# Kernel optimization log

Hardware: AMD Instinct MI355X
Metric: run time of the kernel (lower is better)

The kernel has to match this reference:

```python
import jax, jax.numpy as jnp
import numpy as np

T, N, E, IN, HID, H, DK, L, OUT = 2, 16384, 262144, 128, 256, 8, 32, 2, 64
SRC_T, DST_T = (0, 1), (1, 0)
SQRT_DK = float(np.sqrt(DK))


def _gelu(x):
    return jax.nn.gelu(x, approximate=False)


def _seg_softmax(scores, seg, n):
    # edge softmax normalized by destination node (variable in-degree segments)
    m = jax.ops.segment_max(scores, seg, num_segments=n)
    e = jnp.exp(scores - m[seg])
    d = jax.ops.segment_sum(e, seg, num_segments=n)
    return e / d[seg]


def _posvect(x, ww, wb, lw, lb, sw, sb, gw, gb, fw, fb):
    # x: [T,N,6] scalar features; per-(type,modality) weights [T,6,HID]; fw: [T,6,4*HID,HID]
    xe = x[..., None]                                    # [T,N,6,1]
    aff = lambda w, b: xe * w[:, None] + b[:, None]      # [T,N,6,HID]
    acts = (jnp.sin(aff(ww, wb)), aff(lw, lb),
            jax.nn.softplus(aff(sw, sb)), jax.nn.sigmoid(aff(gw, gb)))
    out = fb[:, None]
    for i, a in enumerate(acts):
        out = out + jnp.einsum('tnmh,tmhk->tnmk', a, fw[:, :, i * HID:(i + 1) * HID, :])
    return out                                           # [T,N,6,HID]


def _forward(node_ft, scalars, src_idx, dst_idx, proj_w, proj_b,
             pv_wave_w, pv_wave_b, pv_lin_w, pv_lin_b, pv_sp_w, pv_sp_b,
             pv_sig_w, pv_sig_b, pv_fc_w, pv_fc_b, ima_w1, ima_b1, ima_w2,
             lyr_k_w, lyr_q_w, lyr_v_w, lyr_fc_w, lyr_k_b, lyr_q_b, lyr_v_b,
             lyr_fc_b, lyr_att_w, lyr_val_w, lyr_canon, lyr_res,
             lyr_ln_g, lyr_ln_b, out_w, out_b, sel_node_type):
    # per-type input projection + six positional encodings -> 7 modalities
    h0 = _gelu(jnp.einsum('tnd,tdh->tnh', node_ft, proj_w) + proj_b[:, None])
    pv = _gelu(_posvect(scalars, pv_wave_w, pv_wave_b, pv_lin_w, pv_lin_b,
                        pv_sp_w, pv_sp_b, pv_sig_w, pv_sig_b, pv_fc_w, pv_fc_b))
    z = jnp.concatenate([h0[:, :, None], pv], axis=2)    # [T,N,7,HID]
    w = jnp.tanh(z @ ima_w1 + ima_b1) @ ima_w2           # [T,N,7,1]
    h = (jax.nn.softmax(w, axis=2) * z).sum(2)           # [T,N,HID]
    for l in range(L):
        k = (jnp.einsum('tnd,tdh->tnh', h, lyr_k_w[l]) + lyr_k_b[l][:, None]).reshape(T, N, H, DK)
        q = (jnp.einsum('tnd,tdh->tnh', h, lyr_q_w[l]) + lyr_q_b[l][:, None]).reshape(T, N, H, DK)
        v = (jnp.einsum('tnd,tdh->tnh', h, lyr_v_w[l]) + lyr_v_b[l][:, None]).reshape(T, N, H, DK)
        agg = [None, None]
        for e in range(2):  # canonical etypes: (a->b), (b->a)
            st, dt = SRC_T[e], DST_T[e]
            ke = jnp.einsum('nhi,hij->nhj', k[st], lyr_att_w[l, e])
            ve = jnp.einsum('nhi,hij->nhj', v[st], lyr_val_w[l, e])
            s, d = src_idx[e], dst_idx[e]
            score = (q[dt][d] * ke[s]).sum(-1) * lyr_canon[l, e] / SQRT_DK  # [E,H]
            attn = _seg_softmax(score, d, N)
            agg[dt] = jax.ops.segment_sum(ve[s] * attn[..., None], d, num_segments=N)
        t = jnp.stack(agg).reshape(T, N, HID)  # cross_reducer mean over single etype per dst == identity
        alpha = jax.nn.sigmoid(lyr_res[l])[:, None, None]
        hp = jnp.einsum('tnh,thk->tnk', t, lyr_fc_w[l]) + lyr_fc_b[l][:, None]
        hp = hp * alpha + h * (1.0 - alpha)
        mu = hp.mean(-1, keepdims=True)
        var = ((hp - mu) ** 2).mean(-1, keepdims=True)
        h = (hp - mu) / jnp.sqrt(var + 1e-5) * lyr_ln_g[l][:, None] + lyr_ln_b[l][:, None]
    return h[sel_node_type] @ out_w + out_b


def setup_inputs() -> dict:
    key = jax.random.key(0)
    ks = iter(jax.random.split(key, 64))
    nrm = lambda shape, scale=1.0: jax.random.normal(next(ks), shape, dtype=jnp.float32) * scale
    inp = {}
    inp['node_ft'] = nrm((T, N, IN))
    inp['scalars'] = jax.random.uniform(next(ks), (T, N, 6), dtype=jnp.float32)
    inp['src_idx'] = jax.random.randint(next(ks), (T, E), 0, N, dtype=jnp.int32)
    inp['dst_idx'] = jax.random.randint(next(ks), (T, E), 0, N, dtype=jnp.int32)
    inp['proj_w'] = nrm((T, IN, HID), IN ** -0.5)
    inp['proj_b'] = jnp.zeros((T, HID), jnp.float32)
    for nm in ['pv_wave_w', 'pv_wave_b', 'pv_lin_w', 'pv_lin_b', 'pv_sp_w', 'pv_sp_b', 'pv_sig_w', 'pv_sig_b']:
        inp[nm] = nrm((T, 6, HID))
    inp['pv_fc_w'] = nrm((T, 6, 4 * HID, HID), (4 * HID) ** -0.5)
    inp['pv_fc_b'] = jnp.zeros((T, 6, HID), jnp.float32)
    inp['ima_w1'] = nrm((HID, 128), HID ** -0.5)
    inp['ima_b1'] = jnp.zeros((128,), jnp.float32)
    inp['ima_w2'] = nrm((128, 1), 128 ** -0.5)
    for nm in ['lyr_k_w', 'lyr_q_w', 'lyr_v_w', 'lyr_fc_w']:
        inp[nm] = nrm((L, T, HID, HID), HID ** -0.5)
    for nm in ['lyr_k_b', 'lyr_q_b', 'lyr_v_b', 'lyr_fc_b']:
        inp[nm] = jnp.zeros((L, T, HID), jnp.float32)
    inp['lyr_att_w'] = nrm((L, 2, H, DK, DK), DK ** -0.5)
    inp['lyr_val_w'] = nrm((L, 2, H, DK, DK), DK ** -0.5)
    inp['lyr_canon'] = jnp.ones((L, 2, H), jnp.float32)
    inp['lyr_res'] = jnp.ones((L, T), jnp.float32)
    inp['lyr_ln_g'] = jnp.ones((L, T, HID), jnp.float32)
    inp['lyr_ln_b'] = jnp.zeros((L, T, HID), jnp.float32)
    inp['out_w'] = nrm((HID, OUT), HID ** -0.5)
    inp['out_b'] = jnp.zeros((OUT,), jnp.float32)
    inp['sel_node_type'] = 0
    return inp


def reference(node_ft, scalars, src_idx, dst_idx, proj_w, proj_b,
              pv_wave_w, pv_wave_b, pv_lin_w, pv_lin_b, pv_sp_w, pv_sp_b,
              pv_sig_w, pv_sig_b, pv_fc_w, pv_fc_b, ima_w1, ima_b1, ima_w2,
              lyr_k_w, lyr_q_w, lyr_v_w, lyr_fc_w, lyr_k_b, lyr_q_b, lyr_v_b,
              lyr_fc_b, lyr_att_w, lyr_val_w, lyr_canon, lyr_res,
              lyr_ln_g, lyr_ln_b, out_w, out_b, sel_node_type):
    return _forward(node_ft, scalars, src_idx, dst_idx, proj_w, proj_b,
                    pv_wave_w, pv_wave_b, pv_lin_w, pv_lin_b, pv_sp_w, pv_sp_b,
                    pv_sig_w, pv_sig_b, pv_fc_w, pv_fc_b, ima_w1, ima_b1, ima_w2,
                    lyr_k_w, lyr_q_w, lyr_v_w, lyr_fc_w, lyr_k_b, lyr_q_b, lyr_v_b,
                    lyr_fc_b, lyr_att_w, lyr_val_w, lyr_canon, lyr_res,
                    lyr_ln_g, lyr_ln_b, out_w, out_b, sel_node_type)
```

## Files before the change

### kernel.cpp

```cpp
#include <hip/hip_runtime.h>
#include <hip/hip_bf16.h>

typedef unsigned short u16;
typedef unsigned int   u32;
typedef __attribute__((ext_vector_type(8))) short bf16x8;
typedef __attribute__((ext_vector_type(4))) float f32x4;
typedef __attribute__((ext_vector_type(4))) u16   u16x4;

constexpr int TT  = 2;
constexpr int NN  = 16384;
constexpr int EE  = 262144;

__device__ __forceinline__ u16 f2b(float f){
  u32 x = __float_as_uint(f);
  u32 r = (x + 0x7fffu + ((x >> 16) & 1u)) >> 16;
  return (u16)r;
}
__device__ __forceinline__ float b2f(u16 u){ return __uint_as_float(((u32)u) << 16); }
__device__ __forceinline__ u32 pack2bf(float a, float b){
  __hip_bfloat162 h = __float22bfloat162_rn(make_float2(a, b));
  union { __hip_bfloat162 h2; u32 u; } cv; cv.h2 = h; return cv.u;
}

__device__ __forceinline__ int swz64(int row, int c){
  return (row << 6) + (c ^ ((row & 7) << 3));
}

__device__ __forceinline__ void gl_lds16(const u16* g, u16* l){
  __builtin_amdgcn_global_load_lds(
      (const __attribute__((address_space(1))) u32*)g,
      (__attribute__((address_space(3))) u32*)l, 16, 0, 0);
}

__device__ __forceinline__ float fast_tanh(float u){
  return 1.f - 2.f*__builtin_amdgcn_rcpf(1.f + __expf(2.f*u));
}
__device__ __forceinline__ float gelu_f(float x){
  float u = 0.7978845608028654f * (x + 0.044715f * x*x*x);
  return 0.5f * x * (1.f + fast_tanh(u));
}

__global__ void csr_hist(const int* __restrict__ dst, int* __restrict__ cnt){
  int id = blockIdx.x*256 + threadIdx.x;
  int e = id >> 18;
  atomicAdd(&cnt[e*NN + dst[id]], 1);
}

__global__ void csr_scan(const int* __restrict__ cnt, int* __restrict__ offs){
  const int e = blockIdx.x, tid = threadIdx.x;
  const int CH = NN/256;
  const int* c = cnt + e*NN;
  int* of = offs + e*(NN+1);
  const int base = tid*CH;
  int s = 0;
  for(int i=0;i<CH;i++) s += c[base+i];
  __shared__ int sm[256];
  sm[tid] = s; __syncthreads();
  for(int o=1;o<256;o<<=1){
    int v = (tid>=o) ? sm[tid-o] : 0;
    __syncthreads();
    sm[tid] += v;
    __syncthreads();
  }
  int run = sm[tid] - s;
  for(int i=0;i<CH;i++){ of[base+i] = run; run += c[base+i]; }
  if(tid==255) of[NN] = run;
}

__global__ void csr_scatter(const int* __restrict__ dst, const int* __restrict__ src,
                            const int* __restrict__ offs, int* __restrict__ cur,
                            int* __restrict__ elist){
  int id = blockIdx.x*256 + threadIdx.x;
  int e = id >> 18;
  int d = dst[id];
  int pos = offs[e*(NN+1)+d] + atomicAdd(&cur[e*NN+d], 1);
  elist[e*EE + pos] = src[id];
}

__global__ void tconv(const float* __restrict__ in, u16* __restrict__ out, int K, int Nc){
  __shared__ float tile[32][33];
  const long base = (long)blockIdx.z * K * Nc;
  const int k0 = blockIdx.x*32, n0 = blockIdx.y*32;
  const int tx = threadIdx.x, ty = threadIdx.y;
  for(int i=0;i<32;i+=8)
    tile[ty+i][tx] = in[base + (long)(k0+ty+i)*Nc + n0+tx];
  __syncthreads();
  for(int i=0;i<32;i+=8)
    out[base + (long)(n0+ty+i)*K + k0+tx] = f2b(tile[tx][ty+i]);
}

__global__ void eff_w(const float* __restrict__ kw, const float* __restrict__ vw,
                      const float* __restrict__ kb, const float* __restrict__ vb,
                      const float* __restrict__ att, const float* __restrict__ val,
                      u16* __restrict__ qkvwt, float* __restrict__ qkvb){
  const int h = blockIdx.x, lt = blockIdx.y, kv = blockIdx.z;
  const int l = lt >> 1;
  const float* W = (kv ? vw : kw) + (long)lt*65536;
  const float* A = (kv ? val : att) + (long)lt*8192 + h*1024;
  const float* B = (kv ? vb : kb) + (long)lt*256 + h*32;
  __shared__ float As[32][33];
  for(int idx=threadIdx.x; idx<1024; idx+=256) As[idx>>5][idx&31] = A[idx];
  __syncthreads();
  const int r = threadIdx.x;
  float x[32];
  const float* wr = W + (long)r*256 + h*32;
  #pragma unroll
  for(int i=0;i<32;i++) x[i] = wr[i];
  u16* outb = qkvwt + (kv ? 524288 : 0) + (long)lt*65536;
  #pragma unroll 4
  for(int j=0;j<32;j++){
    float s = 0.f;
    #pragma unroll
    for(int i=0;i<32;i++) s = fmaf(x[i], As[i][j], s);
    outb[(h*32 + j)*256 + r] = f2b(s);
  }
  if (r < 32){
    float s = 0.f;
    #pragma unroll
    for(int i=0;i<32;i++) s = fmaf(B[i], As[i][r], s);
    qkvb[l*1536 + (kv ? 1024 : 0) + (lt&1)*256 + h*32 + r] = s;
  }
}

__global__ void pack_qb(const float* __restrict__ qb, float* __restrict__ qkvb){
  int i = blockIdx.x*256 + threadIdx.x;
  int l = i >> 9, r = i & 511;
  qkvb[l*1536 + 512 + r] = qb[l*512 + r];
}

__global__ void cheb_g(const float* __restrict__ ww, const float* __restrict__ wb,
                       const float* __restrict__ lw, const float* __restrict__ lb,
                       const float* __restrict__ sw, const float* __restrict__ sb,
                       const float* __restrict__ gw, const float* __restrict__ gb,
                       const float* __restrict__ fcw, float* __restrict__ Gpart){
  const int p  = blockIdx.x;
  const int by = blockIdx.y;
  const int zg = blockIdx.z;
  const int s  = p >> 1;
  const int tid = threadIdx.x;
  __shared__ float as_[128][9];
  if (tid < 128){
    const int hl = (p & 1)*128 + tid;
    const float* W = (s==0 ? ww : s==1 ? lw : s==2 ? sw : gw) + by*256;
    const float* B = (s==0 ? wb : s==1 ? lb : s==2 ? sb : gb) + by*256;
    const float w = W[hl], b = B[hl];
    #pragma unroll
    for (int dd=0; dd<8; dd++){
      const int d = zg*8 + dd;
      const float th = ((float)d + 0.5f) * (3.14159265358979323846f/32.f);
      const float x  = 0.5f*cosf(th) + 0.5f;
      const float y  = x*w + b;
      float a;
      if (s==0)      a = sinf(y);
      else if (s==1) a = y;
      else if (s==2) a = fmaxf(y,0.f) + log1pf(expf(-fabsf(y)));
      else           a = 1.f/(1.f + expf(-y));
      as_[tid][dd] = a;
    }
  }
  __syncthreads();
  const int k = tid;
  float acc[8];
  #pragma unroll
  for (int dd=0; dd<8; dd++) acc[dd] = 0.f;
  const float* fwp = fcw + ((long)by*1024 + p*128)*256 + k;
  for (int hh=0; hh<128; hh++){
    const float f = fwp[(long)hh*256];
    #pragma unroll
    for (int dd=0; dd<8; dd++) acc[dd] = fmaf(as_[hh][dd], f, acc[dd]);
  }
  float* gp = Gpart + (long)(by*8 + p)*32*256 + (long)(zg*8)*256 + k;
  #pragma unroll
  for (int dd=0; dd<8; dd++) gp[dd*256] = acc[dd];
}

__global__ void cheb_dct(const float* __restrict__ Gpart, const float* __restrict__ fcb,
                         u16* __restrict__ Cbf, float* __restrict__ c0b){
  const int by = blockIdx.x; const int k = threadIdx.x;
  __shared__ float ct[1024];
  for (int i=k; i<1024; i+=256){
    const int j = i>>5, d = i&31;
    ct[i] = cosf((float)j*((float)d + 0.5f)*(3.14159265358979323846f/32.f));
  }
  __syncthreads();
  float g[32];
  #pragma unroll
  for (int d=0; d<32; d++){
    float s = 0.f;
    #pragma unroll
    for (int p=0; p<8; p++) s += Gpart[(long)(by*8+p)*32*256 + d*256 + k];
    g[d] = s;
  }
  u16* co = Cbf + ((long)by*256 + k)*32;
  #pragma unroll
  for (int j=0; j<32; j++){
    float s = 0.f;
    #pragma unroll
    for (int d=0; d<32; d++) s = fmaf(g[d], ct[j*32+d], s);
    if (j==0){ c0b[by*256+k] = s*(1.f/32.f) + fcb[by*256+k]; co[0] = 0; }
    else co[j] = f2b(s*(1.f/16.f));
  }
}

__global__ void __launch_bounds__(256,2)
posvect2(const float* __restrict__ scalars, const u16* __restrict__ Cbf,
         const float* __restrict__ c0b, u16* __restrict__ zb){
  __shared__ __align__(16) u16 lB[256*40];
  __shared__ float xs[128];
  const int tid = threadIdx.x;
  const int by = blockIdx.y;
  const int t = by / 6, m = by % 6;
  const int m0 = blockIdx.x * 128;
  const int lane = tid & 63, wvi = tid >> 6;
  const int wc0 = wvi * 64;
  const int l16 = lane & 15, qd = lane >> 4;

  if (tid < 128) xs[tid] = scalars[((long)t*NN + m0 + tid)*6 + m];
  const u16* Cb = Cbf + (long)by*8192;
  for (int idx = tid; idx < 1024; idx += 256){
    const int row = idx >> 2, ch = idx & 3;
    *(uint4*)&lB[row*40 + ch*8] = *(const uint4*)&Cb[row*32 + ch*8];
  }
  __syncthreads();

  bf16x8 af[8];
  #pragma unroll
  for (int i=0;i<8;i++){
    const float u = 2.f*xs[i*16 + l16] - 1.f;
    float t0 = 1.f, t1 = u;
    u32 pk[16];
    pk[0] = pack2bf(t0, t1);
    #pragma unroll
    for (int j2=1; j2<16; j2++){
      const float a = 2.f*u*t1 - t0;
      const float b = 2.f*u*a  - t1;
      pk[j2] = pack2bf(a, b);
      t0 = a; t1 = b;
    }
    u32 w[4];
    #pragma unroll
    for (int c=0;c<4;c++){
      const u32 v01 = (qd & 2) ? pk[8+c]  : pk[c];
      const u32 v23 = (qd & 2) ? pk[12+c] : pk[4+c];
      w[c] = (qd & 1) ? v23 : v01;
    }
    union { u32 u4[4]; bf16x8 v; } cv;
    cv.u4[0]=w[0]; cv.u4[1]=w[1]; cv.u4[2]=w[2]; cv.u4[3]=w[3];
    af[i] = cv.v;
  }

  bf16x8 bfr[4];
  #pragma unroll
  for (int jj=0;jj<4;jj++)
    bfr[jj] = *(const bf16x8*)&lB[(wc0 + jj*16 + l16)*40 + qd*8];

  f32x4 acc[8][4];
  #pragma unroll
  for (int i=0;i<8;i++)
    #pragma unroll
    for (int jj=0;jj<4;jj++)
      acc[i][jj] = __builtin_amdgcn_mfma_f32_16x16x32_bf16(
          af[i], bfr[jj], (f32x4){0.f,0.f,0.f,0.f}, 0,0,0);

  float bvj[4];
  #pragma unroll
  for (int jj=0;jj<4;jj++) bvj[jj] = c0b[by*256 + wc0 + jj*16 + l16];

  u16* st = (u16*)lB;
  u16* zout = zb + ((long)t*NN + m0)*1792 + (m+1)*256;
  #pragma unroll
  for (int c=0;c<4;c++){
    __syncthreads();
    #pragma unroll
    for (int ii=0;ii<2;ii++){
      const int i = c*2 + ii;
      #pragma unroll
      for (int jj=0;jj<4;jj++){
        const int col = wc0 + jj*16 + l16;
        #pragma unroll
        for (int r=0;r<4;r++){
          const int rowl = ii*16 + qd*4 + r;
          st[rowl*264 + col] = f2b(gelu_f(acc[i][jj][r] + bvj[jj]));
        }
      }
    }
    __syncthreads();
    #pragma unroll
    for (int it=0; it<4; it++){
      const int f = it*256 + tid;
      const int rowl = f >> 5, seg = f & 31;
      const uint4 v = *(const uint4*)&st[rowl*264 + seg*8];
      *(uint4*)&zout[(long)(c*32 + rowl)*1792 + seg*8] = v;
    }
  }
}

template<int BM,int BN,int BK,int WM,int WN,int ASRC,int EPI,int ZQKV>
__global__ void __launch_bounds__(256,2)
gemm_k(const void* __restrict__ Av, const u16* __restrict__ Bt,
       const float* __restrict__ bias, void* Cv,
       int K, int lda, int ldc,
       long strideA, long strideB, long strideBias, long strideC,
       const float* resid, const float* __restrict__ resgate,
       const int* __restrict__ selp, u16* __restrict__ kvout,
       const float* __restrict__ lng, const float* __restrict__ lnb)
{
  static_assert(BK == 64, "swizzle assumes BK=64");
  constexpr int WTM = BM/WM, WTN = BN/WN;
  constexpr int RM = WTM/16, RN = WTN/16;
  __shared__ __align__(16) u16 lA[BM*64];
  __shared__ __align__(16) u16 lB[BN*64];

  const int tid = threadIdx.x;
  const int by  = blockIdx.y;
  const int m0  = blockIdx.x * BM;
  const int lane = tid & 63, wvi = tid >> 6;
  const int wr = wvi / WN, wc = wvi % WN;
  const int wr0 = wr * WTM, wc0 = wc * WTN;
  const int l16 = lane & 15, qd = lane >> 4;
  const int csrc = (((lane & 7) ^ (lane >> 3)) << 3);

  int zq = 0; int boff = 0;
  if constexpr (ZQKV){
    zq = blockIdx.z;
    boff = zq*512;
  }

  long aoff = (long)by * strideA;
  if (selp) aoff += (long)selp[0] * strideA;
  const float* A32 = (const float*)Av;
  const u16*   A16 = (const u16*)Av;
  const u16*   Bp  = Bt + (long)by * strideB + (long)zq * 262144;

  f32x4 acc[RM][RN];
  #pragma unroll
  for(int i=0;i<RM;i++)
    #pragma unroll
    for(int j=0;j<RN;j++) acc[i][j] = (f32x4){0.f,0.f,0.f,0.f};

  for(int k0=0;k0<K;k0+=BK){
    if constexpr (ASRC == 0){
      for(int idx=tid; idx < BM*16; idx += 256){
        int r = idx >> 4, c = (idx & 15)*4;
        const float4 v = *(const float4*)(A32 + aoff + (long)(m0+r)*lda + k0 + c);
        uint2 o2; o2.x = pack2bf(v.x, v.y); o2.y = pack2bf(v.z, v.w);
        *(uint2*)&lA[swz64(r, c)] = o2;
      }
    } else {
      #pragma unroll
      for(int ch = wvi; ch < BM/8; ch += 4){
        const int r = ch*8 + (lane>>3);
        gl_lds16(A16 + aoff + (long)(m0+r)*lda + k0 + csrc, &lA[ch*512]);
      }
    }
    #pragma unroll
    for(int ch = wvi; ch < BN/8; ch += 4){
      const int n = ch*8 + (lane>>3);
      gl_lds16(Bp + (long)n*K + k0 + csrc, &lB[ch*512]);
    }
    __syncthreads();
    #pragma unroll
    for(int ks=0; ks<BK; ks+=32){
      bf16x8 af[RM], bfr[RN];
      #pragma unroll
      for(int i=0;i<RM;i++) af[i]  = *(const bf16x8*)&lA[swz64(wr0 + i*16 + l16, ks + qd*8)];
      #pragma unroll
      for(int j=0;j<RN;j++) bfr[j] = *(const bf16x8*)&lB[swz64(wc0 + j*16 + l16, ks + qd*8)];
      #pragma unroll
      for(int i=0;i<RM;i++)
        #pragma unroll
        for(int j=0;j<RN;j++)
          acc[i][j] = __builtin_amdgcn_mfma_f32_16x16x32_bf16(af[i], bfr[j], acc[i][j], 0,0,0);
    }
    __syncthreads();
  }

  if constexpr (EPI == 4){
    float* rsum = (float*)lA;
    #pragma unroll
    for(int i=0;i<RM;i++){
      #pragma unroll
      for(int r=0;r<4;r++){
        float part = 0.f;
        #pragma unroll
        for(int jj=0;jj<RN;jj++){
          const int col = wc0 + jj*16 + l16;
          const float v = fast_tanh(acc[i][jj][r] + bias[boff + col]);
          part += v * resid[col];
        }
        part += __shfl_xor(part,1); part += __shfl_xor(part,2);
        part += __shfl_xor(part,4); part += __shfl_xor(part,8);
        if (l16 == 0) rsum[wc*BM + wr0 + i*16 + qd*4 + r] = part;
      }
    }
    __syncthreads();
    if (tid < BM){
      float s = 0.f;
      #pragma unroll
      for(int w=0;w<WN;w++) s += rsum[w*BM + tid];
      ((float*)Cv)[m0 + tid] = s;
    }
    return;
  } else if constexpr (EPI == 5){
    float* red1 = (float*)lA;
    float* red2 = red1 + WN*BM;
    float* muv  = red2 + WN*BM;
    const float alpha = 1.f/(1.f + __expf(-resgate[by]));
    #pragma unroll
    for(int i=0;i<RM;i++){
      #pragma unroll
      for(int r=0;r<4;r++){
        const int rloc = wr0 + i*16 + qd*4 + r;
        const int row = m0 + rloc;
        float s1 = 0.f, s2 = 0.f;
        #pragma unroll
        for(int j=0;j<RN;j++){
          const int col = wc0 + j*16 + l16;
          float v = acc[i][j][r] + bias[(long)by*strideBias + col];
          const float hv = resid[(long)by*strideC + (long)row*ldc + col];
          v = v*alpha + hv*(1.f - alpha);
          acc[i][j][r] = v;
          s1 += v; s2 += v*v;
        }
        s1 += __shfl_xor(s1,1); s1 += __shfl_xor(s1,2); s1 += __shfl_xor(s1,4); s1 += __shfl_xor(s1,8);
        s2 += __shfl_xor(s2,1); s2 += __shfl_xor(s2,2); s2 += __shfl_xor(s2,4); s2 += __shfl_xor(s2,8);
        if (l16 == 0){ red1[wc*BM + rloc] = s1; red2[wc*BM + rloc] = s2; }
      }
    }
    __syncthreads();
    if (tid < BM){
      float s1 = 0.f, s2 = 0.f;
      #pragma unroll
      for(int w=0;w<WN;w++){ s1 += red1[w*BM + tid]; s2 += red2[w*BM + tid]; }
      const float mu = s1*(1.f/256.f);
      const float var = s2*(1.f/256.f) - mu*mu;
      muv[tid*2]   = mu;
      muv[tid*2+1] = rsqrtf(fmaxf(var, 0.f) + 1e-5f);
    }
    __syncthreads();
    #pragma unroll
    for(int i=0;i<RM;i++){
      #pragma unroll
      for(int r=0;r<4;r++){
        const int rloc = wr0 + i*16 + qd*4 + r;
        const int row = m0 + rloc;
        const float mu = muv[rloc*2], rs = muv[rloc*2+1];
        #pragma unroll
        for(int j=0;j<RN;j++){
          const int col = wc0 + j*16 + l16;
          const float o = (acc[i][j][r]-mu)*rs*lng[by*256+col] + lnb[by*256+col];
          ((float*)Cv)[(long)by*strideC + (long)row*ldc + col] = o;
        }
      }
    }
    return;
  } else {
    #pragma unroll
    for(int i=0;i<RM;i++){
      #pragma unroll
      for(int j=0;j<RN;j++){
        const int col = wc0 + j*16 + l16;
        const float bv = bias[(long)by*strideBias + boff + col];
        #pragma unroll
        for(int r=0;r<4;r++){
          const int row = m0 + wr0 + i*16 + qd*4 + r;
          float v = acc[i][j][r] + bv;
          if constexpr (ZQKV){
            if (zq == 1)
              ((u16*)Cv)[(long)by*strideC + (long)row*ldc + col] = f2b(v);
            else
              kvout[((long)by*NN + row)*512 + ((col>>2)<<3) + (zq==2 ? 4 : 0) + (col&3)] = f2b(v);
          } else {
            const long cidx = (long)by*strideC + (long)row*ldc + col;
            if constexpr (EPI == 0) ((float*)Cv)[cidx] = v;
            else ((u16*)Cv)[cidx] = f2b(gelu_f(v));
          }
        }
      }
    }
  }
}

__global__ void ima_combine(const u16* __restrict__ zb, const float* __restrict__ wbuf,
                            float* __restrict__ H){
  const int row = blockIdx.x*4 + (threadIdx.x>>6);
  const int lane = threadIdx.x & 63;
  const float* w7 = wbuf + (long)row*7;
  float w[7]; float mx = -1e30f;
  #pragma unroll
  for(int m=0;m<7;m++){ w[m] = w7[m]; mx = fmaxf(mx, w[m]); }
  float sum = 0.f;
  #pragma unroll
  for(int m=0;m<7;m++){ w[m] = __expf(w[m]-mx); sum += w[m]; }
  const float inv = __builtin_amdgcn_rcpf(sum);
  float4 acc = {0,0,0,0};
  #pragma unroll
  for(int m=0;m<7;m++){
    const u16x4 z4 = *(const u16x4*)&zb[((long)row*7 + m)*256 + lane*4];
    const float p = w[m]*inv;
    acc.x += p*b2f(z4.x); acc.y += p*b2f(z4.y); acc.z += p*b2f(z4.z); acc.w += p*b2f(z4.w);
  }
  *(float4*)&H[(long)row*256 + lane*4] = acc;
}

__global__ void attn_agg(const u16* __restrict__ Q16, const u16* __restrict__ KV,
                         u16* __restrict__ AGG,
                         const int* __restrict__ offs, const int* __restrict__ elist,
                         const float* __restrict__ canon){
  const int e = blockIdx.y, dt = 1 - e;
  const int d = blockIdx.x*4 + (threadIdx.x>>6);
  const int lane = threadIdx.x & 63;
  const float scale = canon[e*8 + (lane>>3)] * 0.17677669529663687f;

  const uint2 qv = *(const uint2*)&Q16[((long)dt*NN + d)*256 + lane*4];
  const float q0 = b2f((u16)(qv.x&0xffff)), q1 = b2f((u16)(qv.x>>16));
  const float q2 = b2f((u16)(qv.y&0xffff)), q3 = b2f((u16)(qv.y>>16));

  const int p0 = offs[e*(NN+1) + d], p1 = offs[e*(NN+1) + d + 1];
  const int* el = elist + (long)e*EE;
  const u16* KVb = KV + (long)e*NN*512;

  float a0=0.f, a1=0.f, a2=0.f, a3=0.f;
  float den = 0.f;

  auto process = [&](const uint4 kv){
    float dp = q0*b2f((u16)(kv.x&0xffff)) + q1*b2f((u16)(kv.x>>16))
             + q2*b2f((u16)(kv.y&0xffff)) + q3*b2f((u16)(kv.y>>16));
    dp += __shfl_xor(dp,1); dp += __shfl_xor(dp,2); dp += __shfl_xor(dp,4);
    const float w = __expf(dp*scale);
    den += w;
    a0 = fmaf(w, b2f((u16)(kv.z&0xffff)), a0);
    a1 = fmaf(w, b2f((u16)(kv.z>>16)),    a1);
    a2 = fmaf(w, b2f((u16)(kv.w&0xffff)), a2);
    a3 = fmaf(w, b2f((u16)(kv.w>>16)),    a3);
  };

  int p = p0;
  for(; p+8 <= p1; p += 8){
    uint4 kv[8];
    #pragma unroll
    for(int u=0;u<8;u++) kv[u] = *(const uint4*)&KVb[(long)el[p+u]*512 + lane*8];
    #pragma unroll
    for(int u=0;u<8;u++) process(kv[u]);
  }
  for(; p+2 <= p1; p += 2){
    const uint4 a = *(const uint4*)&KVb[(long)el[p]*512 + lane*8];
    const uint4 b = *(const uint4*)&KVb[(long)el[p+1]*512 + lane*8];
    process(a); process(b);
  }
  if (p < p1){
    const uint4 a = *(const uint4*)&KVb[(long)el[p]*512 + lane*8];
    process(a);
  }

  uint2 o = {0,0};
  if (p1 > p0){
    const float r = 1.f/den;
    o.x = pack2bf(a0*r, a1*r);
    o.y = pack2bf(a2*r, a3*r);
  }
  *(uint2*)&AGG[((long)dt*NN + d)*256 + lane*4] = o;
}

extern "C" void kernel_launch(void* const* d_in, const int* in_sizes, int n_in,
                              void* d_out, int out_size, void* d_ws, size_t ws_size,
                              hipStream_t stream) {
  const float* node_ft = (const float*)d_in[0];
  const float* scalars = (const float*)d_in[1];
  const int*   src_idx = (const int*)d_in[2];
  const int*   dst_idx = (const int*)d_in[3];
  const float* proj_w  = (const float*)d_in[4];
  const float* proj_b  = (const float*)d_in[5];
  const float* pv_ww   = (const float*)d_in[6];
  const float* pv_wb   = (const float*)d_in[7];
  const float* pv_lw   = (const float*)d_in[8];
  const float* pv_lb   = (const float*)d_in[9];
  const float* pv_sw   = (const float*)d_in[10];
  const float* pv_sb   = (const float*)d_in[11];
  const float* pv_gw   = (const float*)d_in[12];
  const float* pv_gb   = (const float*)d_in[13];
  const float* pv_fcw  = (const float*)d_in[14];
  const float* pv_fcb  = (const float*)d_in[15];
  const float* ima_w1  = (const float*)d_in[16];
  const float* ima_b1  = (const float*)d_in[17];
  const float* ima_w2  = (const float*)d_in[18];
  const float* lyr_k_w = (const float*)d_in[19];
  const float* lyr_q_w = (const float*)d_in[20];
  const float* lyr_v_w = (const float*)d_in[21];
  const float* lyr_fc_w= (const float*)d_in[22];
  const float* lyr_k_b = (const float*)d_in[23];
  const float* lyr_q_b = (const float*)d_in[24];
  const float* lyr_v_b = (const float*)d_in[25];
  const float* lyr_fc_b= (const float*)d_in[26];
  const float* lyr_att_w=(const float*)d_in[27];
  const float* lyr_val_w=(const float*)d_in[28];
  const float* lyr_canon=(const float*)d_in[29];
  const float* lyr_res = (const float*)d_in[30];
  const float* lyr_ln_g= (const float*)d_in[31];
  const float* lyr_ln_b= (const float*)d_in[32];
  const float* out_w   = (const float*)d_in[33];
  const float* out_b   = (const float*)d_in[34];
  const int*   sel     = (const int*)d_in[35];
  float* outp = (float*)d_out;

  char* ws = (char*)d_ws;
  size_t o = 0;
  auto alloc = [&](size_t bytes)->char*{ char* p = ws + o; o = (o + bytes + 255) & ~(size_t)255; return p; };

  int*   cnt    = (int*)  alloc(2*NN*4);
  int*   cur    = (int*)  alloc(2*NN*4);
  int*   offs   = (int*)  alloc(2*(NN+1)*4);
  int*   elist  = (int*)  alloc(2*EE*4);
  u16*   projwt = (u16*)  alloc((size_t)TT*128*256*2);
  u16*   imaw1t = (u16*)  alloc((size_t)256*128*2);
  u16*   qkvwt  = (u16*)  alloc((size_t)3*262144*2);
  u16*   fcwt   = (u16*)  alloc((size_t)4*256*256*2);
  u16*   outwt  = (u16*)  alloc((size_t)64*256*2);
  float* hbuf   = (float*)alloc((size_t)TT*NN*256*4);
  float* wbuf   = (float*)alloc((size_t)TT*NN*7*4);
  float* Gpart  = (float*)alloc((size_t)12*8*32*256*4);
  u16*   Cbf    = (u16*)  alloc((size_t)12*256*32*2);
  float* c0b    = (float*)alloc((size_t)12*256*4);
  float* qkvb   = (float*)alloc((size_t)TT*3*2*256*4);
  char*  arena  = alloc((size_t)176160768);
  if (o > ws_size) return;

  u16*   zbuf  = (u16*)arena;
  u16*   Qb16  = (u16*)arena;
  u16*   KVb   = (u16*)(arena + 16777216);
  u16*   AGG16 = (u16*)(arena + 50331648);

  hipMemsetAsync(cnt, 0, 2*NN*4, stream);
  hipMemsetAsync(cur, 0, 2*NN*4, stream);
  csr_hist   <<<2*EE/256, 256, 0, stream>>>(dst_idx, cnt);
  csr_scan   <<<2, 256, 0, stream>>>(cnt, offs);
  csr_scatter<<<2*EE/256, 256, 0, stream>>>(dst_idx, src_idx, offs, cur, elist);

  tconv<<<dim3( 4,8, 2), dim3(32,8), 0, stream>>>(proj_w,   projwt, 128, 256);
  tconv<<<dim3( 8,4, 1), dim3(32,8), 0, stream>>>(ima_w1,   imaw1t, 256, 128);
  tconv<<<dim3( 8,8, 4), dim3(32,8), 0, stream>>>(lyr_q_w,  qkvwt + 262144, 256, 256);
  tconv<<<dim3( 8,8, 4), dim3(32,8), 0, stream>>>(lyr_fc_w, fcwt,   256, 256);
  tconv<<<dim3( 8,2, 1), dim3(32,8), 0, stream>>>(out_w,    outwt,  256, 64);
  eff_w<<<dim3(8,4,2), 256, 0, stream>>>(lyr_k_w, lyr_v_w, lyr_k_b, lyr_v_b,
                                         lyr_att_w, lyr_val_w, qkvwt, qkvb);
  pack_qb<<<4, 256, 0, stream>>>(lyr_q_b, qkvb);

  cheb_g  <<<dim3(8,12,4), 256, 0, stream>>>(pv_ww, pv_wb, pv_lw, pv_lb,
                                             pv_sw, pv_sb, pv_gw, pv_gb, pv_fcw, Gpart);
  cheb_dct<<<12, 256, 0, stream>>>(Gpart, pv_fcb, Cbf, c0b);

  gemm_k<64,256,64,1,4,0,1,0><<<dim3(256,TT), 256, 0, stream>>>(
      node_ft, projwt, proj_b, zbuf, 128, 128, 1792,
      (long)NN*128, 32768L, 256L, (long)NN*1792, nullptr, nullptr, nullptr, nullptr,
      nullptr, nullptr);

  posvect2<<<dim3(128,12), 256, 0, stream>>>(scalars, Cbf, c0b, zbuf);

  gemm_k<64,128,64,2,2,1,4,0><<<dim3(3584,1), 256, 0, stream>>>(
      zbuf, imaw1t, ima_b1, wbuf, 256, 256, 0,
      0L, 0L, 0L, 0L, ima_w2, nullptr, nullptr, nullptr, nullptr, nullptr);
  ima_combine<<<TT*NN/4, 256, 0, stream>>>(zbuf, wbuf, hbuf);

  for (int l = 0; l < 2; ++l){
    gemm_k<64,256,64,1,4,0,0,1><<<dim3(256,TT,3), 256, 0, stream>>>(
        hbuf, qkvwt + (size_t)l*131072, qkvb + (size_t)l*1536, Qb16, 256, 256, 256,
        (long)NN*256, 65536L, 256L, (long)NN*256, nullptr, nullptr, nullptr, KVb,
        nullptr, nullptr);

    attn_agg<<<dim3(NN/4, 2), 256, 0, stream>>>(Qb16, KVb, AGG16, offs, elist,
                                                lyr_canon + l*2*8);

    gemm_k<64,256,64,1,4,1,5,0><<<dim3(256,TT), 256, 0, stream>>>(
        AGG16, fcwt + (size_t)l*2*65536, lyr_fc_b + l*2*256, hbuf, 256, 256, 256,
        (long)NN*256, 65536L, 256L, (long)NN*256, hbuf, lyr_res + l*2, nullptr, nullptr,
        lyr_ln_g + l*2*256, lyr_ln_b + l*2*256);
  }

  gemm_k<256,64,64,4,1,0,0,0><<<dim3(64,1), 256, 0, stream>>>(
      hbuf, outwt, out_b, outp, 256, 256, 64,
      (long)NN*256, 0L, 0L, 0L, nullptr, nullptr, sel, nullptr, nullptr, nullptr);

  (void)in_sizes; (void)n_in; (void)out_size;
}
```

Baseline: 661.9 us.

## Interleave K/V weight columns at pack time and use one-wave attention blocks

The K and V effective weights and biases are now written in an interleaved column order during weight packing, so the QKV GEMM epilogue stores KV contiguously instead of scattering each column through an index remap. Weights are regrouped per (layer,type) as [K|V|Q], and Q moves to z=2. The aggregation kernel is relaunched with one 64-thread wave per destination node instead of four waves per block, aiming for finer-grained scheduling of variable-degree nodes. Risk: bias and weight index remapping must match exactly, and smaller blocks add launch and occupancy overhead.

```diff
diff --git a/kernel.cpp b/kernel.cpp
--- a/kernel.cpp
+++ b/kernel.cpp
@@ -77,16 +77,18 @@
   elist[e*EE + pos] = src[id];
 }
 
-__global__ void tconv(const float* __restrict__ in, u16* __restrict__ out, int K, int Nc){
+__global__ void tconv(const float* __restrict__ in, u16* __restrict__ out, int K, int Nc,
+                      long ozstride){
   __shared__ float tile[32][33];
-  const long base = (long)blockIdx.z * K * Nc;
+  const long ibase = (long)blockIdx.z * K * Nc;
+  const long obase = (long)blockIdx.z * ozstride;
   const int k0 = blockIdx.x*32, n0 = blockIdx.y*32;
   const int tx = threadIdx.x, ty = threadIdx.y;
   for(int i=0;i<32;i+=8)
-    tile[ty+i][tx] = in[base + (long)(k0+ty+i)*Nc + n0+tx];
+    tile[ty+i][tx] = in[ibase + (long)(k0+ty+i)*Nc + n0+tx];
   __syncthreads();
   for(int i=0;i<32;i+=8)
-    out[base + (long)(n0+ty+i)*K + k0+tx] = f2b(tile[tx][ty+i]);
+    out[obase + (long)(n0+ty+i)*K + k0+tx] = f2b(tile[tx][ty+i]);
 }
 
 __global__ void eff_w(const float* __restrict__ kw, const float* __restrict__ vw,
@@ -106,26 +108,30 @@
   const float* wr = W + (long)r*256 + h*32;
   #pragma unroll
   for(int i=0;i<32;i++) x[i] = wr[i];
-  u16* outb = qkvwt + (kv ? 524288 : 0) + (long)lt*65536;
+  u16* outb = qkvwt + (long)lt*196608;
   #pragma unroll 4
   for(int j=0;j<32;j++){
     float s = 0.f;
     #pragma unroll
     for(int i=0;i<32;i++) s = fmaf(x[i], As[i][j], s);
-    outb[(h*32 + j)*256 + r] = f2b(s);
+    const int c = h*32 + j;
+    const int mc = ((c>>2)<<3) + kv*4 + (c&3);
+    outb[(long)mc*256 + r] = f2b(s);
   }
   if (r < 32){
     float s = 0.f;
     #pragma unroll
     for(int i=0;i<32;i++) s = fmaf(B[i], As[i][r], s);
-    qkvb[l*1536 + (kv ? 1024 : 0) + (lt&1)*256 + h*32 + r] = s;
+    const int c = h*32 + r;
+    const int mc = ((c>>2)<<3) + kv*4 + (c&3);
+    qkvb[l*1536 + (lt&1)*512 + mc] = s;
   }
 }
 
 __global__ void pack_qb(const float* __restrict__ qb, float* __restrict__ qkvb){
   int i = blockIdx.x*256 + threadIdx.x;
   int l = i >> 9, r = i & 511;
-  qkvb[l*1536 + 512 + r] = qb[l*512 + r];
+  qkvb[l*1536 + 1024 + r] = qb[l*512 + r];
 }
 
 __global__ void cheb_g(const float* __restrict__ ww, const float* __restrict__ wb,
@@ -320,17 +326,14 @@
   const int l16 = lane & 15, qd = lane >> 4;
   const int csrc = (((lane & 7) ^ (lane >> 3)) << 3);
 
-  int zq = 0; int boff = 0;
-  if constexpr (ZQKV){
-    zq = blockIdx.z;
-    boff = zq*512;
-  }
+  int zq = 0;
+  if constexpr (ZQKV) zq = blockIdx.z;
 
   long aoff = (long)by * strideA;
   if (selp) aoff += (long)selp[0] * strideA;
   const float* A32 = (const float*)Av;
   const u16*   A16 = (const u16*)Av;
-  const u16*   Bp  = Bt + (long)by * strideB + (long)zq * 262144;
+  const u16*   Bp  = Bt + (long)by * strideB + (long)zq * 65536;
 
   f32x4 acc[RM][RN];
   #pragma unroll
@@ -385,7 +388,7 @@
         #pragma unroll
         for(int jj=0;jj<RN;jj++){
           const int col = wc0 + jj*16 + l16;
-          const float v = fast_tanh(acc[i][jj][r] + bias[boff + col]);
+          const float v = fast_tanh(acc[i][jj][r] + bias[col]);
           part += v * resid[col];
         }
         part += __shfl_xor(part,1); part += __shfl_xor(part,2);
@@ -460,16 +463,20 @@
       #pragma unroll
       for(int j=0;j<RN;j++){
         const int col = wc0 + j*16 + l16;
-        const float bv = bias[(long)by*strideBias + boff + col];
+        float bv;
+        if constexpr (ZQKV)
+          bv = bias[(zq==2) ? (1024 + (long)by*256 + col) : ((long)by*512 + zq*256 + col)];
+        else
+          bv = bias[(long)by*strideBias + col];
         #pragma unroll
         for(int r=0;r<4;r++){
           const int row = m0 + wr0 + i*16 + qd*4 + r;
           float v = acc[i][j][r] + bv;
           if constexpr (ZQKV){
-            if (zq == 1)
+            if (zq == 2)
               ((u16*)Cv)[(long)by*strideC + (long)row*ldc + col] = f2b(v);
             else
-              kvout[((long)by*NN + row)*512 + ((col>>2)<<3) + (zq==2 ? 4 : 0) + (col&3)] = f2b(v);
+              kvout[((long)by*NN + row)*512 + zq*256 + col] = f2b(v);
           } else {
             const long cidx = (long)by*strideC + (long)row*ldc + col;
             if constexpr (EPI == 0) ((float*)Cv)[cidx] = v;
@@ -503,13 +510,14 @@
   *(float4*)&H[(long)row*256 + lane*4] = acc;
 }
 
-__global__ void attn_agg(const u16* __restrict__ Q16, const u16* __restrict__ KV,
-                         u16* __restrict__ AGG,
-                         const int* __restrict__ offs, const int* __restrict__ elist,
-                         const float* __restrict__ canon){
+__global__ void __launch_bounds__(64)
+attn_agg(const u16* __restrict__ Q16, const u16* __restrict__ KV,
+         u16* __restrict__ AGG,
+         const int* __restrict__ offs, const int* __restrict__ elist,
+         const float* __restrict__ canon){
   const int e = blockIdx.y, dt = 1 - e;
-  const int d = blockIdx.x*4 + (threadIdx.x>>6);
-  const int lane = threadIdx.x & 63;
+  const int d = blockIdx.x;
+  const int lane = threadIdx.x;
   const float scale = canon[e*8 + (lane>>3)] * 0.17677669529663687f;
 
   const uint2 qv = *(const uint2*)&Q16[((long)dt*NN + d)*256 + lane*4];
@@ -613,7 +621,7 @@
   int*   elist  = (int*)  alloc(2*EE*4);
   u16*   projwt = (u16*)  alloc((size_t)TT*128*256*2);
   u16*   imaw1t = (u16*)  alloc((size_t)256*128*2);
-  u16*   qkvwt  = (u16*)  alloc((size_t)3*262144*2);
+  u16*   qkvwt  = (u16*)  alloc((size_t)4*196608*2);
   u16*   fcwt   = (u16*)  alloc((size_t)4*256*256*2);
   u16*   outwt  = (u16*)  alloc((size_t)64*256*2);
   float* hbuf   = (float*)alloc((size_t)TT*NN*256*4);
@@ -636,11 +644,11 @@
   csr_scan   <<<2, 256, 0, stream>>>(cnt, offs);
   csr_scatter<<<2*EE/256, 256, 0, stream>>>(dst_idx, src_idx, offs, cur, elist);
 
-  tconv<<<dim3( 4,8, 2), dim3(32,8), 0, stream>>>(proj_w,   projwt, 128, 256);
-  tconv<<<dim3( 8,4, 1), dim3(32,8), 0, stream>>>(ima_w1,   imaw1t, 256, 128);
-  tconv<<<dim3( 8,8, 4), dim3(32,8), 0, stream>>>(lyr_q_w,  qkvwt + 262144, 256, 256);
-  tconv<<<dim3( 8,8, 4), dim3(32,8), 0, stream>>>(lyr_fc_w, fcwt,   256, 256);
-  tconv<<<dim3( 8,2, 1), dim3(32,8), 0, stream>>>(out_w,    outwt,  256, 64);
+  tconv<<<dim3( 4,8, 2), dim3(32,8), 0, stream>>>(proj_w,   projwt, 128, 256, 32768L);
+  tconv<<<dim3( 8,4, 1), dim3(32,8), 0, stream>>>(ima_w1,   imaw1t, 256, 128, 32768L);
+  tconv<<<dim3( 8,8, 4), dim3(32,8), 0, stream>>>(lyr_q_w,  qkvwt + 131072, 256, 256, 196608L);
+  tconv<<<dim3( 8,8, 4), dim3(32,8), 0, stream>>>(lyr_fc_w, fcwt,   256, 256, 65536L);
+  tconv<<<dim3( 8,2, 1), dim3(32,8), 0, stream>>>(out_w,    outwt,  256, 64, 16384L);
   eff_w<<<dim3(8,4,2), 256, 0, stream>>>(lyr_k_w, lyr_v_w, lyr_k_b, lyr_v_b,
                                          lyr_att_w, lyr_val_w, qkvwt, qkvb);
   pack_qb<<<4, 256, 0, stream>>>(lyr_q_b, qkvb);
@@ -663,12 +671,12 @@
 
   for (int l = 0; l < 2; ++l){
     gemm_k<64,256,64,1,4,0,0,1><<<dim3(256,TT,3), 256, 0, stream>>>(
-        hbuf, qkvwt + (size_t)l*131072, qkvb + (size_t)l*1536, Qb16, 256, 256, 256,
-        (long)NN*256, 65536L, 256L, (long)NN*256, nullptr, nullptr, nullptr, KVb,
+        hbuf, qkvwt + (size_t)l*393216, qkvb + (size_t)l*1536, Qb16, 256, 256, 256,
+        (long)NN*256, 196608L, 0L, (long)NN*256, nullptr, nullptr, nullptr, KVb,
         nullptr, nullptr);
 
-    attn_agg<<<dim3(NN/4, 2), 256, 0, stream>>>(Qb16, KVb, AGG16, offs, elist,
-                                                lyr_canon + l*2*8);
+    attn_agg<<<dim3(NN, 2), 64, 0, stream>>>(Qb16, KVb, AGG16, offs, elist,
+                                             lyr_canon + l*2*8);
 
     gemm_k<64,256,64,1,4,1,5,0><<<dim3(256,TT), 256, 0, stream>>>(
         AGG16, fcwt + (size_t)l*2*65536, lyr_fc_b + l*2*256, hbuf, 256, 256, 256,
```

Result: slower. 738.9 us (+11.6%).
